# Performance work log

Measured on AMD Instinct MI355X. Metric: run time of the kernel, lower is better.

Reference implementation:

```python
import jax, jax.numpy as jnp
import numpy as np

NUM_HEADS = 8
EPS = 1e-12  # torch F.normalize default eps


def conv1x1(x, w):
    # x: [b,c,h,w], w: [o,c]
    return jnp.einsum('bchw,oc->bohw', x, w)


def dwconv3x3(x, w):
    # depthwise 3x3, w: [c,1,3,3]
    return jax.lax.conv_general_dilated(
        x, w, window_strides=(1, 1), padding=((1, 1), (1, 1)),
        dimension_numbers=('NCHW', 'OIHW', 'NCHW'),
        feature_group_count=x.shape[1])


def l2norm(x):
    n = jnp.sqrt(jnp.sum(x * x, axis=-1, keepdims=True))
    return x / jnp.maximum(n, EPS)


def channel_attn(q, k, v, temperature, b, c, h, w):
    hd = c // NUM_HEADS
    q = l2norm(q.reshape(b, NUM_HEADS, hd, h * w))
    k = l2norm(k.reshape(b, NUM_HEADS, hd, h * w))
    v = v.reshape(b, NUM_HEADS, hd, h * w)
    attn = jnp.einsum('bndl,bnel->bnde', q, k) * temperature  # [b,nh,hd,hd]
    attn = jax.nn.softmax(attn, axis=-1)
    out = jnp.einsum('bnde,bnel->bndl', attn, v)
    return out.reshape(b, c, h, w)


def fdfp(x, w1, w2, h, w):
    xf = jnp.fft.rfft2(x, norm='ortho')  # over last two axes
    xfreq = jnp.concatenate([xf.real, xf.imag], axis=1)
    xfreq = conv1x1(xfreq, w1)
    xfreq = jax.nn.gelu(xfreq, approximate=False)
    xfreq = conv1x1(xfreq, w2)
    c2 = xfreq.shape[1] // 2
    xc = jax.lax.complex(xfreq[:, :c2], xfreq[:, c2:])
    return jnp.fft.irfft2(xc, s=(h, w), norm='ortho')


def setup_inputs() -> dict:
    key = jax.random.key(0)
    ks = jax.random.split(key, 10)
    dim = 192
    b, h, w = 4, 128, 128
    s = 0.05
    return {
        'x': jax.random.normal(ks[0], (b, dim, h, w), jnp.float32),
        'w_qkv1': jax.random.normal(ks[1], (3 * dim, dim), jnp.float32) * s,
        'w_qkv1_dw': jax.random.normal(ks[2], (3 * dim, 1, 3, 3), jnp.float32) * s,
        'w_proj1': jax.random.normal(ks[3], (dim, dim), jnp.float32) * s,
        'w_fdfp1': jax.random.normal(ks[4], (2 * dim, 2 * dim), jnp.float32) * s,
        'w_fdfp2': jax.random.normal(ks[5], (2 * dim, 2 * dim), jnp.float32) * s,
        'w_kv2': jax.random.normal(ks[6], (2 * dim, dim), jnp.float32) * s,
        'w_kv2_dw': jax.random.normal(ks[7], (2 * dim, 1, 3, 3), jnp.float32) * s,
        'w_proj2': jax.random.normal(ks[8], (dim, dim), jnp.float32) * s,
        'temperature': jnp.ones((NUM_HEADS, 1, 1), jnp.float32),
    }


def reference(x, w_qkv1, w_qkv1_dw, w_proj1, w_fdfp1, w_fdfp2,
              w_kv2, w_kv2_dw, w_proj2, temperature):
    b, c, h, w = x.shape
    # Stage 1: spatial-domain transposed (channel) attention
    qkv1 = dwconv3x3(conv1x1(x, w_qkv1), w_qkv1_dw)
    q1, k1, v1 = jnp.split(qkv1, 3, axis=1)
    out1 = channel_attn(q1, k1, v1, temperature, b, c, h, w)
    out1 = conv1x1(out1, w_proj1)
    # Stage 2: frequency-domain query, spatial K/V from stage-1 output
    q2 = fdfp(x, w_fdfp1, w_fdfp2, h, w)
    kv2 = dwconv3x3(conv1x1(out1, w_kv2), w_kv2_dw)
    k2, v2 = jnp.split(kv2, 2, axis=1)
    out2 = channel_attn(q2, k2, v2, temperature, b, c, h, w)
    out2 = conv1x1(out2, w_proj2)
    return out2
```

## Files before the change

kernel.cpp:

```cpp
#include <hip/hip_runtime.h>
#include <math.h>

typedef _Float16 half_t;
typedef half_t h8v __attribute__((ext_vector_type(8)));
typedef half_t h4v __attribute__((ext_vector_type(4)));
typedef float f32x4 __attribute__((ext_vector_type(4)));

namespace {
constexpr int DIMC = 192;
constexpr int NB = 4;
constexpr int HH = 128, WW = 128;
constexpr int HW = HH * WW;
constexpr int NH = 8, HD = 24;
constexpr int FP = 80;
constexpr long LT_PART = 128L * 192 * FP;
constexpr long LT_B    = 2 * LT_PART;
constexpr long LT_ROW  = 192L * FP;
constexpr long XB  = 192L * HW;
constexpr long CB0 = 0;
constexpr long CB1 = 15728640;
constexpr long OFF_T1 = 37748736;
constexpr long OFF_Q2 = 50331648;
constexpr long OFF_S  = 62914560;
constexpr long OFF_KT = 0;
constexpr long OFF_KF = 25165824;
constexpr long OFF_O2 = 0;
constexpr int  GSL = 64;
constexpr long SM_INVQ1 = OFF_S;
constexpr long SM_INVK1 = OFF_S + 768;
constexpr long SM_INVQ2 = OFF_S + 1536;
constexpr long SM_INVK2 = OFF_S + 2304;
constexpr long SM_ATT   = OFF_S + 3072;
constexpr long H0       = OFF_S + 168960;
constexpr long H_WQKV = H0;
constexpr long H_WF   = H0 + 55296;
constexpr long H_W1   = H0 + 92160;
constexpr long H_W2   = H0 + 165888;
constexpr long H_PRJ  = H0 + 239616;
constexpr long H_B2   = H0 + 258048;
constexpr long H_B3   = H0 + 290816;
constexpr long H_B1T  = H0 + 323584;
constexpr long H_B4T  = H0 + 333824;
constexpr float PI2 = 6.283185307179586476f;
}

__global__ void cvt16_k(const float* __restrict__ in, half_t* __restrict__ o, int n) {
    int i = blockIdx.x * 256 + threadIdx.x;
    if (i < n) o[i] = (half_t)in[i];
}
__global__ void initB1t_k(half_t* __restrict__ B) {
    int idx = blockIdx.x * 256 + threadIdx.x;
    if (idx >= 160 * 128) return;
    int j = idx / 128, k = idx % 128;
    float v = 0.f;
    if (j < 65) v = cosf(PI2 * ((k * j) & 127) / 128.f) * (1.f / 128.f);
    else if (j >= 80 && j < 145) v = -sinf(PI2 * ((k * (j - 80)) & 127) / 128.f) * (1.f / 128.f);
    B[idx] = (half_t)v;
}
__global__ void initB2h_k(half_t* __restrict__ B) {
    int idx = blockIdx.x * 256 + threadIdx.x;
    int m = idx >> 8, cin = idx & 255;
    int pd = m >> 7, ky = m & 127;
    int ps = cin >> 7, y = cin & 127;
    float c, s; sincosf(PI2 * ((ky * y) & 127) / 128.f, &s, &c);
    float v = (pd == 0) ? (ps == 0 ? c : s) : (ps == 0 ? -s : c);
    B[idx] = (half_t)v;
}
__global__ void initB3h_k(half_t* __restrict__ B) {
    int idx = blockIdx.x * 256 + threadIdx.x;
    int m = idx >> 8, cin = idx & 255;
    int pd = m >> 7, y = m & 127;
    int ps = cin >> 7, ky = cin & 127;
    float c, s; sincosf(PI2 * ((y * ky) & 127) / 128.f, &s, &c);
    float v = (pd == 0) ? (ps == 0 ? c : -s) : (ps == 0 ? s : c);
    B[idx] = (half_t)v;
}
__global__ void initB4t_k(half_t* __restrict__ B) {
    int idx = blockIdx.x * 256 + threadIdx.x;
    if (idx >= 128 * 160) return;
    int j = idx / 160, k = idx % 160;
    float v = 0.f;
    if (k < 80) {
        if (k == 0) v = 1.f / 128.f;
        else if (k < 64) v = 2.f * cosf(PI2 * ((k * j) & 127) / 128.f) / 128.f;
        else if (k == 64) v = cosf(PI2 * ((64 * j) & 127) / 128.f) / 128.f;
    } else {
        int kx = k - 80;
        if (kx >= 1 && kx < 64) v = -2.f * sinf(PI2 * ((kx * j) & 127) / 128.f) / 128.f;
    }
    B[idx] = (half_t)v;
}
__global__ void fusew_k(const float* __restrict__ wkv, const float* __restrict__ wproj,
                        half_t* __restrict__ wf) {
    int o = blockIdx.x, c = threadIdx.x;
    float acc = 0.f;
    for (int m = 0; m < 192; ++m) acc += wkv[o * 192 + m] * wproj[m * 192 + c];
    wf[o * 192 + c] = (half_t)acc;
}

template<int PFOLD, int GELU>
__global__ __launch_bounds__(256) void k2m(
    const half_t* __restrict__ W16, int Cin,
    const float* __restrict__ X, long xBatch, int iSplit, long iLo, long iHi,
    float* __restrict__ out, long oBatch, int oSplit, long oLo, long oHi) {
    __shared__ __align__(16) half_t Wh[64 * 40];
    __shared__ __align__(16) half_t Xh[256 * 40];
    const int t = threadIdx.x;
    const int o0 = blockIdx.x * 64;
    const long p0 = (long)blockIdx.y * 256;
    const long xb = (long)blockIdx.z * xBatch;
    const long ob = (long)blockIdx.z * oBatch;
    const int lane = t & 63, wv = t >> 6;
    const int fr = lane & 15, fg = lane >> 4;
    const int so = t >> 2, scg = (t & 3) * 8;
    f32x4 acc[4][4];
#pragma unroll
    for (int m = 0; m < 4; ++m)
#pragma unroll
        for (int n = 0; n < 4; ++n) acc[m][n] = {0.f, 0.f, 0.f, 0.f};
    long pa;
    {
        long p = p0 + t;
        if (PFOLD) { long q = p / 80; pa = q * LT_ROW + (p - q * 80); } else pa = p;
    }
    for (int k0 = 0; k0 < Cin; k0 += 32) {
        __syncthreads();
        *(h8v*)&Wh[so * 40 + scg] =
            *(const h8v*)(W16 + (long)(o0 + so) * Cin + k0 + scg);
#pragma unroll
        for (int s = 0; s < 2; ++s) {
            int cb = k0 + s * 16;
            long rb = (cb < iSplit) ? (long)cb * iLo : (long)(cb - iSplit) * iLo + iHi;
            const float* g = X + xb + rb + pa;
            float v[16];
#pragma unroll
            for (int j = 0; j < 16; ++j) v[j] = g[(long)j * iLo];
            h8v h0, h1;
#pragma unroll
            for (int j = 0; j < 8; ++j) { h0[j] = (half_t)v[j]; h1[j] = (half_t)v[8 + j]; }
            *(h8v*)&Xh[t * 40 + s * 16] = h0;
            *(h8v*)&Xh[t * 40 + s * 16 + 8] = h1;
        }
        __syncthreads();
        h8v a[4], bb[4];
#pragma unroll
        for (int m = 0; m < 4; ++m) a[m] = *(const h8v*)&Wh[(m * 16 + fr) * 40 + fg * 8];
#pragma unroll
        for (int n = 0; n < 4; ++n) bb[n] = *(const h8v*)&Xh[(wv * 64 + n * 16 + fr) * 40 + fg * 8];
#pragma unroll
        for (int m = 0; m < 4; ++m)
#pragma unroll
            for (int n = 0; n < 4; ++n)
                acc[m][n] = __builtin_amdgcn_mfma_f32_16x16x32_f16(a[m], bb[n], acc[m][n], 0, 0, 0);
    }
    long pe[4];
#pragma unroll
    for (int n = 0; n < 4; ++n) {
        long p = p0 + wv * 64 + n * 16 + fr;
        if (PFOLD) { long q = p / 80; pe[n] = q * LT_ROW + (p - q * 80); } else pe[n] = p;
    }
#pragma unroll
    for (int m = 0; m < 4; ++m)
#pragma unroll
        for (int i = 0; i < 4; ++i) {
            int o = o0 + m * 16 + fg * 4 + i;
            long oadr = ob + ((o < oSplit) ? (long)o * oLo : (long)(o - oSplit) * oLo + oHi);
#pragma unroll
            for (int n = 0; n < 4; ++n) {
                float v = acc[m][n][i];
                if (GELU) v = 0.5f * v * (1.f + erff(v * 0.70710678118654752f));
                out[oadr + pe[n]] = v;
            }
        }
}

__global__ __launch_bounds__(256) void kff2(
    const half_t* __restrict__ W1, const half_t* __restrict__ W2,
    const float* __restrict__ X, float* __restrict__ out) {
    __shared__ __align__(16) half_t Xh[32 * 40];
    __shared__ __align__(16) half_t Yh[32 * 392];
    const int t = threadIdx.x;
    const long p0 = (long)blockIdx.x * 32;
    const long xb = (long)blockIdx.y * LT_B;
    const int lane = t & 63, wv = t >> 6;
    const int fr = lane & 15, fg = lane >> 4;
    const int sp = t & 31;
    const int skb = (t >> 5) * 4;
    long pa;
    { long p = p0 + sp; long q = p / 80; pa = q * LT_ROW + (p - q * 80); }
    f32x4 acc[6][2];
#pragma unroll
    for (int m = 0; m < 6; ++m)
#pragma unroll
        for (int n = 0; n < 2; ++n) acc[m][n] = {0.f, 0.f, 0.f, 0.f};

    for (int k0 = 0; k0 < 384; k0 += 32) {
        __syncthreads();
        {
            int c0 = k0 + skb;
            long rb = (c0 < 192) ? (long)c0 * 80 : (long)(c0 - 192) * 80 + LT_PART;
            const float* g = X + xb + rb + pa;
            h4v h;
#pragma unroll
            for (int j = 0; j < 4; ++j) h[j] = (half_t)g[(long)j * 80];
            *(h4v*)&Xh[sp * 40 + skb] = h;
        }
        __syncthreads();
        h8v a[6], bb[2];
#pragma unroll
        for (int m = 0; m < 6; ++m)
            a[m] = *(const h8v*)(W1 + (long)(wv * 96 + m * 16 + fr) * 384 + k0 + fg * 8);
#pragma unroll
        for (int n = 0; n < 2; ++n) bb[n] = *(const h8v*)&Xh[(n * 16 + fr) * 40 + fg * 8];
#pragma unroll
        for (int m = 0; m < 6; ++m)
#pragma unroll
            for (int n = 0; n < 2; ++n)
                acc[m][n] = __builtin_amdgcn_mfma_f32_16x16x32_f16(a[m], bb[n], acc[m][n], 0, 0, 0);
    }
#pragma unroll
    for (int m = 0; m < 6; ++m)
#pragma unroll
        for (int n = 0; n < 2; ++n) {
            int o4 = wv * 96 + m * 16 + fg * 4;
            int p = n * 16 + fr;
            h4v h;
#pragma unroll
            for (int i = 0; i < 4; ++i) {
                float v = acc[m][n][i];
                v = 0.5f * v * (1.f + erff(v * 0.70710678118654752f));
                h[i] = (half_t)v;
            }
            *(h4v*)&Yh[p * 392 + o4] = h;
        }
#pragma unroll
    for (int m = 0; m < 6; ++m)
#pragma unroll
        for (int n = 0; n < 2; ++n) acc[m][n] = {0.f, 0.f, 0.f, 0.f};
    __syncthreads();

    for (int k0 = 0; k0 < 384; k0 += 32) {
        h8v a[6], bb[2];
#pragma unroll
        for (int m = 0; m < 6; ++m)
            a[m] = *(const h8v*)(W2 + (long)(wv * 96 + m * 16 + fr) * 384 + k0 + fg * 8);
#pragma unroll
        for (int n = 0; n < 2; ++n) bb[n] = *(const h8v*)&Yh[(n * 16 + fr) * 392 + k0 + fg * 8];
#pragma unroll
        for (int m = 0; m < 6; ++m)
#pragma unroll
            for (int n = 0; n < 2; ++n)
                acc[m][n] = __builtin_amdgcn_mfma_f32_16x16x32_f16(a[m], bb[n], acc[m][n], 0, 0, 0);
    }
    long pe[2];
#pragma unroll
    for (int n = 0; n < 2; ++n) {
        long p = p0 + n * 16 + fr;
        long q = p / 80; pe[n] = q * LT_ROW + (p - q * 80);
    }
#pragma unroll
    for (int m = 0; m < 6; ++m)
#pragma unroll
        for (int i = 0; i < 4; ++i) {
            int o = wv * 96 + m * 16 + fg * 4 + i;
            long oadr = xb + ((o < 192) ? (long)o * 80 : (long)(o - 192) * 80 + LT_PART);
#pragma unroll
            for (int n = 0; n < 2; ++n) out[oadr + pe[n]] = acc[m][n][i];
        }
}

template<int NF, int NORM>
__global__ __launch_bounds__(256) void k1m(
    const float* __restrict__ A, long aBatch, long aC, long aRow, int aSplit, long aHiOff, int K,
    const uint* __restrict__ Bt32,
    float* __restrict__ out, long oBatch, long oC, long oRow, int oSplit, long oHiOff,
    float* __restrict__ inv) {
    __shared__ __align__(16) half_t Ah[128 * 40];
    __shared__ __align__(16) half_t Bh[160 * 40];
    const int t = threadIdx.x;
    const long ab = (long)blockIdx.z * aBatch + (long)blockIdx.x * aC;
    const long ob = (long)blockIdx.z * oBatch + (long)blockIdx.x * oC;
    const int N = NF * 32;
    const int lane = t & 63, wv = t >> 6;
    const int wm = wv >> 1, wn = wv & 1;
    const int fr = lane & 15, fg = lane >> 4;
    const int sr = t >> 1, shalf = t & 1;
    const int Kw = K >> 1;
    f32x4 acc[4][NF];
#pragma unroll
    for (int m = 0; m < 4; ++m)
#pragma unroll
        for (int n = 0; n < NF; ++n) acc[m][n] = {0.f, 0.f, 0.f, 0.f};
    for (int k0 = 0; k0 < K; k0 += 32) {
        __syncthreads();
        {
            int cb = k0 + shalf * 16;
            long rb = (cb < aSplit) ? (long)cb : (long)(cb - aSplit) + aHiOff;
            const float* g = A + ab + (long)sr * aRow + rb;
            float4 v0 = *(const float4*)g;
            float4 v1 = *(const float4*)(g + 4);
            float4 v2 = *(const float4*)(g + 8);
            float4 v3 = *(const float4*)(g + 12);
            h8v h0, h1;
            h0[0] = (half_t)v0.x; h0[1] = (half_t)v0.y; h0[2] = (half_t)v0.z; h0[3] = (half_t)v0.w;
            h0[4] = (half_t)v1.x; h0[5] = (half_t)v1.y; h0[6] = (half_t)v1.z; h0[7] = (half_t)v1.w;
            h1[0] = (half_t)v2.x; h1[1] = (half_t)v2.y; h1[2] = (half_t)v2.z; h1[3] = (half_t)v2.w;
            h1[4] = (half_t)v3.x; h1[5] = (half_t)v3.y; h1[6] = (half_t)v3.z; h1[7] = (half_t)v3.w;
            *(h8v*)&Ah[sr * 40 + shalf * 16] = h0;
            *(h8v*)&Ah[sr * 40 + shalf * 16 + 8] = h1;
        }
        for (int j = t; j < N * 16; j += 256) {
            int n = j >> 4, kw = j & 15;
            *(uint*)&Bh[n * 40 + kw * 2] = Bt32[(long)n * Kw + (k0 >> 1) + kw];
        }
        __syncthreads();
        h8v a[4], bb[NF];
#pragma unroll
        for (int m = 0; m < 4; ++m) a[m] = *(const h8v*)&Ah[(wm * 64 + m * 16 + fr) * 40 + fg * 8];
#pragma unroll
        for (int n = 0; n < NF; ++n) bb[n] = *(const h8v*)&Bh[(wn * NF * 16 + n * 16 + fr) * 40 + fg * 8];
#pragma unroll
        for (int m = 0; m < 4; ++m)
#pragma unroll
            for (int n = 0; n < NF; ++n)
                acc[m][n] = __builtin_amdgcn_mfma_f32_16x16x32_f16(a[m], bb[n], acc[m][n], 0, 0, 0);
    }
#pragma unroll
    for (int m = 0; m < 4; ++m)
#pragma unroll
        for (int i = 0; i < 4; ++i) {
            int r = wm * 64 + m * 16 + fg * 4 + i;
            float* orow = out + ob + (long)r * oRow;
#pragma unroll
            for (int n = 0; n < NF; ++n) {
                int j = wn * NF * 16 + n * 16 + fr;
                long jm = (j < oSplit) ? (long)j : (long)(j - oSplit) + oHiOff;
                orow[jm] = acc[m][n][i];
            }
        }
    if (NORM) {
        float ss = 0.f;
#pragma unroll
        for (int m = 0; m < 4; ++m)
#pragma unroll
            for (int n = 0; n < NF; ++n)
#pragma unroll
                for (int i = 0; i < 4; ++i) ss += acc[m][n][i] * acc[m][n][i];
        __syncthreads();
        float* red = (float*)Ah;
        red[t] = ss;
        __syncthreads();
        for (int st = 128; st > 0; st >>= 1) {
            if (t < st) red[t] += red[t + st];
            __syncthreads();
        }
        if (t == 0) inv[(long)blockIdx.z * 192 + blockIdx.x] = 1.f / fmaxf(sqrtf(red[0]), 1e-12f);
    }
}

__global__ __launch_bounds__(256) void dw3_k(
    const float* __restrict__ in, long inBatch,
    const float* __restrict__ w9,
    float* __restrict__ out, long outBatch,
    int normCnt, float* __restrict__ inv) {
    const int c = blockIdx.x, b = blockIdx.y;
    const int t = threadIdx.x;
    const float* ip = in + (long)b * inBatch + (long)c * HW;
    float* op = out + (long)b * outBatch + (long)c * HW;
    const float* wp = w9 + c * 9;
    const float w0 = wp[0], w1 = wp[1], w2 = wp[2];
    const float w3 = wp[3], w4 = wp[4], w5 = wp[5];
    const float w6 = wp[6], w7 = wp[7], w8 = wp[8];
    const int tx = t & 31;
    const int x0 = tx * 4;
    const int y0 = (t >> 5) * 16;
    const bool lx = (tx > 0), rx = (tx < 31);
    float Ar[6], Br[6], Cr[6];
#define LOADROW(Y, R) do { \
        const float* _p = ip + (Y) * 128 + x0; \
        float4 _v = *(const float4*)_p; \
        R[1] = _v.x; R[2] = _v.y; R[3] = _v.z; R[4] = _v.w; \
        R[0] = lx ? _p[-1] : 0.f; \
        R[5] = rx ? _p[4] : 0.f; } while (0)
    if (y0 == 0) { Ar[0]=Ar[1]=Ar[2]=Ar[3]=Ar[4]=Ar[5]=0.f; }
    else LOADROW(y0 - 1, Ar);
    LOADROW(y0, Br);
    float ss = 0.f;
#pragma unroll
    for (int i = 0; i < 16; ++i) {
        int y = y0 + i;
        if (y + 1 < 128) { LOADROW(y + 1, Cr); }
        else { Cr[0]=Cr[1]=Cr[2]=Cr[3]=Cr[4]=Cr[5]=0.f; }
        float o0 = Ar[0]*w0 + Ar[1]*w1 + Ar[2]*w2
                 + Br[0]*w3 + Br[1]*w4 + Br[2]*w5
                 + Cr[0]*w6 + Cr[1]*w7 + Cr[2]*w8;
        float o1 = Ar[1]*w0 + Ar[2]*w1 + Ar[3]*w2
                 + Br[1]*w3 + Br[2]*w4 + Br[3]*w5
                 + Cr[1]*w6 + Cr[2]*w7 + Cr[3]*w8;
        float o2 = Ar[2]*w0 + Ar[3]*w1 + Ar[4]*w2
                 + Br[2]*w3 + Br[3]*w4 + Br[4]*w5
                 + Cr[2]*w6 + Cr[3]*w7 + Cr[4]*w8;
        float o3 = Ar[3]*w0 + Ar[4]*w1 + Ar[5]*w2
                 + Br[3]*w3 + Br[4]*w4 + Br[5]*w5
                 + Cr[3]*w6 + Cr[4]*w7 + Cr[5]*w8;
        *(float4*)(op + y * 128 + x0) = make_float4(o0, o1, o2, o3);
        ss += o0*o0 + o1*o1 + o2*o2 + o3*o3;
#pragma unroll
        for (int j = 0; j < 6; ++j) { Ar[j] = Br[j]; Br[j] = Cr[j]; }
    }
#undef LOADROW
    if (normCnt > 0 && c < normCnt) {
        __shared__ float red[256];
        red[t] = ss;
        __syncthreads();
        for (int st = 128; st > 0; st >>= 1) {
            if (t < st) red[t] += red[t + st];
            __syncthreads();
        }
        if (t == 0) inv[(long)b * 192 + c] = 1.f / fmaxf(sqrtf(red[0]), 1e-12f);
    }
}

__global__ __launch_bounds__(576) void gramf_k(
    const float* __restrict__ q, long qB,
    const float* __restrict__ k, long kB,
    float* __restrict__ gp) {
    __shared__ float qs[HD][260];
    __shared__ float ks[HD][260];
    const int bn = blockIdx.x, ls = blockIdx.y;
    const int b = bn >> 3, n = bn & 7;
    const int t = threadIdx.x;
    const int l0 = ls * 256;
    const float* qp = q + (long)b * qB + (long)(n * HD) * HW + l0;
    const float* kp = k + (long)b * kB + (long)(n * HD) * HW + l0;
    for (int idx = t; idx < HD * 64; idx += 576) {
        int row = idx >> 6, c4 = (idx & 63) * 4;
        *(float4*)&qs[row][c4] = *(const float4*)(qp + (long)row * HW + c4);
        *(float4*)&ks[row][c4] = *(const float4*)(kp + (long)row * HW + c4);
    }
    __syncthreads();
    const int d = t / 24, e = t - d * 24;
    float acc = 0.f;
#pragma unroll 8
    for (int j = 0; j < 256; j += 4) {
        float4 a = *(const float4*)&qs[d][j];
        float4 bb = *(const float4*)&ks[e][j];
        acc += a.x * bb.x + a.y * bb.y + a.z * bb.z + a.w * bb.w;
    }
    gp[((long)bn * 576 + t) * GSL + ls] = acc;
}

__global__ __launch_bounds__(256) void softmax_k(
    const float* __restrict__ gp, const float* __restrict__ invq,
    const float* __restrict__ invk, const float* __restrict__ temp,
    float* __restrict__ attn) {
    int bn = blockIdx.x;
    int b = bn >> 3, n = bn & 7;
    int t = threadIdx.x;
    __shared__ float sums[576];
    for (int idx = t; idx < 576; idx += 256) {
        const float* g = gp + ((long)bn * 576 + idx) * GSL;
        float s = 0.f;
        for (int i = 0; i < GSL; i += 4) {
            float4 v = *(const float4*)(g + i);
            s += v.x + v.y + v.z + v.w;
        }
        sums[idx] = s;
    }
    __syncthreads();
    int d = t;
    if (d >= HD) return;
    float tt = temp[n];
    float iq = invq[b * 192 + n * HD + d];
    float row[HD];
#pragma unroll
    for (int e = 0; e < HD; ++e)
        row[e] = sums[d * HD + e] * iq * invk[b * 192 + n * HD + e] * tt;
    float m = row[0];
#pragma unroll
    for (int e = 1; e < HD; ++e) m = fmaxf(m, row[e]);
    float ssum = 0.f;
#pragma unroll
    for (int e = 0; e < HD; ++e) { row[e] = expf(row[e] - m); ssum += row[e]; }
    float is = 1.f / ssum;
#pragma unroll
    for (int e = 0; e < HD; ++e) attn[(long)bn * 576 + d * HD + e] = row[e] * is;
}

__global__ void attnapply_k(const float* __restrict__ attn, const float* __restrict__ v,
                            long vB, float* __restrict__ out, long outB) {
    int p = blockIdx.x * 256 + threadIdx.x;
    int bn = blockIdx.y;
    int b = bn >> 3, n = bn & 7;
    __shared__ float a[576];
    for (int i = threadIdx.x; i < 576; i += 256) a[i] = attn[(long)bn * 576 + i];
    __syncthreads();
    const float* vp = v + (long)b * vB + (long)(n * HD) * HW + p;
    float acc[HD];
#pragma unroll
    for (int d = 0; d < HD; ++d) acc[d] = 0.f;
    for (int e = 0; e < HD; ++e) {
        float vv = vp[(long)e * HW];
#pragma unroll
        for (int d = 0; d < HD; ++d) acc[d] += a[d * HD + e] * vv;
    }
    float* op = out + (long)b * outB + (long)(n * HD) * HW + p;
#pragma unroll
    for (int d = 0; d < HD; ++d) op[(long)d * HW] = acc[d];
}

extern "C" void kernel_launch(void* const* d_in, const int* in_sizes, int n_in,
                              void* d_out, int out_size, void* d_ws, size_t ws_size,
                              hipStream_t stream) {
    const float* x        = (const float*)d_in[0];
    const float* w_qkv1   = (const float*)d_in[1];
    const float* w_qkv1dw = (const float*)d_in[2];
    const float* w_proj1  = (const float*)d_in[3];
    const float* w_fdfp1  = (const float*)d_in[4];
    const float* w_fdfp2  = (const float*)d_in[5];
    const float* w_kv2    = (const float*)d_in[6];
    const float* w_kv2dw  = (const float*)d_in[7];
    const float* w_proj2  = (const float*)d_in[8];
    const float* temp     = (const float*)d_in[9];
    float* out = (float*)d_out;
    float* ws  = (float*)d_ws;
    dim3 blk(256);
    const int BIG = 1 << 20;

    cvt16_k<<<432, blk, 0, stream>>>(w_qkv1, (half_t*)(ws + H_WQKV), 110592);
    cvt16_k<<<576, blk, 0, stream>>>(w_fdfp1, (half_t*)(ws + H_W1), 147456);
    cvt16_k<<<576, blk, 0, stream>>>(w_fdfp2, (half_t*)(ws + H_W2), 147456);
    cvt16_k<<<144, blk, 0, stream>>>(w_proj2, (half_t*)(ws + H_PRJ), 36864);
    initB1t_k<<<80, blk, 0, stream>>>((half_t*)(ws + H_B1T));
    initB2h_k<<<256, blk, 0, stream>>>((half_t*)(ws + H_B2));
    initB3h_k<<<256, blk, 0, stream>>>((half_t*)(ws + H_B3));
    initB4t_k<<<80, blk, 0, stream>>>((half_t*)(ws + H_B4T));
    fusew_k<<<384, 192, 0, stream>>>(w_kv2, w_proj1, (half_t*)(ws + H_WF));

    k1m<5, 0><<<dim3(192, 1, 4), blk, 0, stream>>>(
        x, XB, (long)HW, 128L, BIG, 0L, 128,
        (const uint*)(ws + H_B1T),
        ws + CB0, LT_B, (long)FP, LT_ROW, 80, LT_PART, nullptr);
    k2m<0, 0><<<dim3(4, 60, 4), blk, 0, stream>>>(
        (const half_t*)(ws + H_B2), 256,
        ws + CB0, LT_B, 128, LT_ROW, LT_PART,
        ws + CB1, LT_B, 128, LT_ROW, LT_PART);
    kff2<<<dim3(320, 4), blk, 0, stream>>>(
        (const half_t*)(ws + H_W1), (const half_t*)(ws + H_W2),
        ws + CB1, ws + CB0);
    k2m<0, 0><<<dim3(4, 60, 4), blk, 0, stream>>>(
        (const half_t*)(ws + H_B3), 256,
        ws + CB0, LT_B, 128, LT_ROW, LT_PART,
        ws + CB1, LT_B, 128, LT_ROW, LT_PART);
    k1m<4, 1><<<dim3(192, 1, 4), blk, 0, stream>>>(
        ws + CB1, LT_B, (long)FP, LT_ROW, 80, LT_PART, 160,
        (const uint*)(ws + H_B4T),
        ws + OFF_Q2, XB, (long)HW, 128L, BIG, 0L, ws + SM_INVQ2);

    for (int ch = 0; ch < 3; ++ch) {
        k2m<0, 0><<<dim3(3, 64, 4), blk, 0, stream>>>(
            (const half_t*)(ws + H_WQKV) + (long)ch * 192 * 192, 192,
            x, XB, BIG, (long)HW, 0L,
            ws + OFF_T1, XB, BIG, (long)HW, 0L);
        dw3_k<<<dim3(192, 4), blk, 0, stream>>>(
            ws + OFF_T1, XB, w_qkv1dw + ch * 192 * 9,
            ws + (long)ch * 192 * HW, (long)576 * HW,
            ch == 2 ? 0 : 192,
            ch == 0 ? ws + SM_INVQ1 : ws + SM_INVK1);
    }
    gramf_k<<<dim3(32, GSL), 576, 0, stream>>>(
        ws, (long)576 * HW, ws + (long)192 * HW, (long)576 * HW, ws + OFF_T1);
    softmax_k<<<32, blk, 0, stream>>>(ws + OFF_T1, ws + SM_INVQ1, ws + SM_INVK1, temp, ws + SM_ATT);
    attnapply_k<<<dim3(64, 32), blk, 0, stream>>>(
        ws + SM_ATT, ws + (long)384 * HW, (long)576 * HW, ws + OFF_T1, XB);

    k2m<0, 0><<<dim3(6, 64, 4), blk, 0, stream>>>(
        (const half_t*)(ws + H_WF), 192,
        ws + OFF_T1, XB, BIG, (long)HW, 0L,
        ws + OFF_KT, (long)384 * HW, BIG, (long)HW, 0L);
    dw3_k<<<dim3(384, 4), blk, 0, stream>>>(
        ws + OFF_KT, (long)384 * HW, w_kv2dw, ws + OFF_KF, (long)384 * HW,
        192, ws + SM_INVK2);

    gramf_k<<<dim3(32, GSL), 576, 0, stream>>>(
        ws + OFF_Q2, XB, ws + OFF_KF, (long)384 * HW, ws + OFF_KT);
    softmax_k<<<32, blk, 0, stream>>>(ws + OFF_KT, ws + SM_INVQ2, ws + SM_INVK2, temp, ws + SM_ATT);
    attnapply_k<<<dim3(64, 32), blk, 0, stream>>>(
        ws + SM_ATT, ws + OFF_KF + (long)192 * HW, (long)384 * HW, ws + OFF_O2, XB);
    k2m<0, 0><<<dim3(3, 64, 4), blk, 0, stream>>>(
        (const half_t*)(ws + H_PRJ), 192,
        ws + OFF_O2, XB, BIG, (long)HW, 0L,
        out, XB, BIG, (long)HW, 0L);
}
```

Measured before the change: 697.4 us.

## Emit FFT row-stage output as fp16 pixel-major layout for frequency MLP

The second FFT stage GEMM now writes its result as fp16 in a [batch, ky, kx, 384-channel] layout, so each frequency point's channels are contiguous. The frequency MLP kernel then reads its B operand straight from global memory as 8-half vectors, with no LDS staging, conversion or barriers in its K loop. This halves the intermediate's bytes and removes strided fp32 gathers. The catch is scattered 2-byte stores in the producer epilogue and uncoalesced-ish direct global operand loads in the consumer.

```diff
diff --git a/kernel.cpp b/kernel.cpp
--- a/kernel.cpp
+++ b/kernel.cpp
@@ -98,7 +98,7 @@
     wf[o * 192 + c] = (half_t)acc;
 }
 
-template<int PFOLD, int GELU>
+template<int PFOLD, int GELU, int OUT16>
 __global__ __launch_bounds__(256) void k2m(
     const half_t* __restrict__ W16, int Cin,
     const float* __restrict__ X, long xBatch, int iSplit, long iLo, long iHi,
@@ -153,6 +153,29 @@
             for (int n = 0; n < 4; ++n)
                 acc[m][n] = __builtin_amdgcn_mfma_f32_16x16x32_f16(a[m], bb[n], acc[m][n], 0, 0, 0);
     }
+    if (OUT16) {
+        half_t* o16 = (half_t*)out;
+        const long bbase = (long)blockIdx.z * 10240;
+        int cN[4], kxN[4];
+#pragma unroll
+        for (int n = 0; n < 4; ++n) {
+            int p = (int)p0 + wv * 64 + n * 16 + fr;
+            int c = p / 80;
+            cN[n] = c; kxN[n] = p - c * 80;
+        }
+#pragma unroll
+        for (int m = 0; m < 4; ++m)
+#pragma unroll
+            for (int i = 0; i < 4; ++i) {
+                int o = o0 + m * 16 + fg * 4 + i;
+                int pd = o >> 7, ky = o & 127;
+#pragma unroll
+                for (int n = 0; n < 4; ++n)
+                    o16[(bbase + ky * 80 + kxN[n]) * 384 + pd * 192 + cN[n]] =
+                        (half_t)acc[m][n][i];
+            }
+        return;
+    }
     long pe[4];
 #pragma unroll
     for (int n = 0; n < 4; ++n) {
@@ -174,44 +197,31 @@
         }
 }
 
-__global__ __launch_bounds__(256) void kff2(
+__global__ __launch_bounds__(256) void kff3(
     const half_t* __restrict__ W1, const half_t* __restrict__ W2,
-    const float* __restrict__ X, float* __restrict__ out) {
-    __shared__ __align__(16) half_t Xh[32 * 40];
+    const half_t* __restrict__ X16, float* __restrict__ out) {
     __shared__ __align__(16) half_t Yh[32 * 392];
     const int t = threadIdx.x;
     const long p0 = (long)blockIdx.x * 32;
     const long xb = (long)blockIdx.y * LT_B;
+    const long x16b = (long)blockIdx.y * 10240;
     const int lane = t & 63, wv = t >> 6;
     const int fr = lane & 15, fg = lane >> 4;
-    const int sp = t & 31;
-    const int skb = (t >> 5) * 4;
-    long pa;
-    { long p = p0 + sp; long q = p / 80; pa = q * LT_ROW + (p - q * 80); }
     f32x4 acc[6][2];
 #pragma unroll
     for (int m = 0; m < 6; ++m)
 #pragma unroll
         for (int n = 0; n < 2; ++n) acc[m][n] = {0.f, 0.f, 0.f, 0.f};
 
+    const half_t* xrow0 = X16 + (x16b + p0 + fr) * 384 + fg * 8;
     for (int k0 = 0; k0 < 384; k0 += 32) {
-        __syncthreads();
-        {
-            int c0 = k0 + skb;
-            long rb = (c0 < 192) ? (long)c0 * 80 : (long)(c0 - 192) * 80 + LT_PART;
-            const float* g = X + xb + rb + pa;
-            h4v h;
-#pragma unroll
-            for (int j = 0; j < 4; ++j) h[j] = (half_t)g[(long)j * 80];
-            *(h4v*)&Xh[sp * 40 + skb] = h;
-        }
-        __syncthreads();
         h8v a[6], bb[2];
 #pragma unroll
         for (int m = 0; m < 6; ++m)
             a[m] = *(const h8v*)(W1 + (long)(wv * 96 + m * 16 + fr) * 384 + k0 + fg * 8);
 #pragma unroll
-        for (int n = 0; n < 2; ++n) bb[n] = *(const h8v*)&Xh[(n * 16 + fr) * 40 + fg * 8];
+        for (int n = 0; n < 2; ++n)
+            bb[n] = *(const h8v*)(xrow0 + (long)(n * 16) * 384 + k0);
 #pragma unroll
         for (int m = 0; m < 6; ++m)
 #pragma unroll
@@ -541,14 +551,14 @@
         x, XB, (long)HW, 128L, BIG, 0L, 128,
         (const uint*)(ws + H_B1T),
         ws + CB0, LT_B, (long)FP, LT_ROW, 80, LT_PART, nullptr);
-    k2m<0, 0><<<dim3(4, 60, 4), blk, 0, stream>>>(
+    k2m<0, 0, 1><<<dim3(4, 60, 4), blk, 0, stream>>>(
         (const half_t*)(ws + H_B2), 256,
         ws + CB0, LT_B, 128, LT_ROW, LT_PART,
-        ws + CB1, LT_B, 128, LT_ROW, LT_PART);
-    kff2<<<dim3(320, 4), blk, 0, stream>>>(
+        ws + CB1, 0L, 0, 0L, 0L);
+    kff3<<<dim3(320, 4), blk, 0, stream>>>(
         (const half_t*)(ws + H_W1), (const half_t*)(ws + H_W2),
-        ws + CB1, ws + CB0);
-    k2m<0, 0><<<dim3(4, 60, 4), blk, 0, stream>>>(
+        (const half_t*)(ws + CB1), ws + CB0);
+    k2m<0, 0, 0><<<dim3(4, 60, 4), blk, 0, stream>>>(
         (const half_t*)(ws + H_B3), 256,
         ws + CB0, LT_B, 128, LT_ROW, LT_PART,
         ws + CB1, LT_B, 128, LT_ROW, LT_PART);
@@ -558,7 +568,7 @@
         ws + OFF_Q2, XB, (long)HW, 128L, BIG, 0L, ws + SM_INVQ2);
 
     for (int ch = 0; ch < 3; ++ch) {
-        k2m<0, 0><<<dim3(3, 64, 4), blk, 0, stream>>>(
+        k2m<0, 0, 0><<<dim3(3, 64, 4), blk, 0, stream>>>(
             (const half_t*)(ws + H_WQKV) + (long)ch * 192 * 192, 192,
             x, XB, BIG, (long)HW, 0L,
             ws + OFF_T1, XB, BIG, (long)HW, 0L);
@@ -574,7 +584,7 @@
     attnapply_k<<<dim3(64, 32), blk, 0, stream>>>(
         ws + SM_ATT, ws + (long)384 * HW, (long)576 * HW, ws + OFF_T1, XB);
 
-    k2m<0, 0><<<dim3(6, 64, 4), blk, 0, stream>>>(
+    k2m<0, 0, 0><<<dim3(6, 64, 4), blk, 0, stream>>>(
         (const half_t*)(ws + H_WF), 192,
         ws + OFF_T1, XB, BIG, (long)HW, 0L,
         ws + OFF_KT, (long)384 * HW, BIG, (long)HW, 0L);
@@ -587,7 +597,7 @@
     softmax_k<<<32, blk, 0, stream>>>(ws + OFF_KT, ws + SM_INVQ2, ws + SM_INVK2, temp, ws + SM_ATT);
     attnapply_k<<<dim3(64, 32), blk, 0, stream>>>(
         ws + SM_ATT, ws + OFF_KF + (long)192 * HW, (long)384 * HW, ws + OFF_O2, XB);
-    k2m<0, 0><<<dim3(3, 64, 4), blk, 0, stream>>>(
+    k2m<0, 0, 0><<<dim3(3, 64, 4), blk, 0, stream>>>(
         (const half_t*)(ws + H_PRJ), 192,
         ws + OFF_O2, XB, BIG, (long)HW, 0L,
         out, XB, BIG, (long)HW, 0L);
```

After: 736.3 us. +5.6%, slower.
